# Kernel tuning notes

Measured on AMD Instinct MI355X. Metric: run time of the kernel, lower is better.

Reference implementation:

```python
import jax, jax.numpy as jnp
import numpy as np

N = 10000      # num_nodes
RP = 16        # latent relations
E = 64         # emb_dim
R = 8000       # num triples (MLP input dim)
NT = 8000      # unique (s,o) pairs (unique by construction)
LW = 64        # lwidth
C = 16         # num_classes
NREL = 50      # num_rels (<= R columns actually used in nhots)


def setup_inputs() -> dict:
    rng = np.random.default_rng(0)
    # unique (s,o) pairs -> nt == R, deterministic shapes
    pair_ids = rng.choice(N * N, size=R, replace=False)
    s = (pair_ids // N).astype(np.int32)
    o = (pair_ids % N).astype(np.int32)
    p = rng.integers(0, NREL, size=R)
    nhots = np.zeros((NT, R), np.float32)
    nhots[np.arange(NT), p] = 1.0
    # replicate index construction from __init__ exactly
    rm = np.arange(RP, dtype=np.int32)[:, None]           # (RP,1)
    s_exp = np.broadcast_to(s[None, :], (RP, NT)).reshape(-1)
    o_exp = np.broadcast_to(o[None, :], (RP, NT)).reshape(-1)
    se = (s[None, :] * rm).reshape(-1)
    oe = (o[None, :] * rm).reshape(-1)
    hindices = np.stack([s_exp, oe], axis=1).astype(np.int32)  # into (N, N*RP)
    vindices = np.stack([se, o_exp], axis=1).astype(np.int32)  # into (N*RP, N)

    key = jax.random.key(0)
    ks = jax.random.split(key, 6)
    inv = lambda d: 1.0 / np.sqrt(d)
    return {
        'nhots': jnp.asarray(nhots),
        'w1a': jax.random.normal(ks[0], (R, LW), jnp.float32) * inv(R),
        'b1a': jnp.zeros((LW,), jnp.float32),
        'w1b': jax.random.normal(ks[1], (LW, RP), jnp.float32) * inv(LW),
        'b1b': jnp.zeros((RP,), jnp.float32),
        'w2a': jax.random.normal(ks[2], (R, LW), jnp.float32) * inv(R),
        'b2a': jnp.zeros((LW,), jnp.float32),
        'w2b': jax.random.normal(ks[3], (LW, RP), jnp.float32) * inv(LW),
        'b2b': jnp.zeros((RP,), jnp.float32),
        'weights1': jax.random.normal(ks[4], (RP, N, E), jnp.float32) * 0.02,
        'bias1': jnp.zeros((E,), jnp.float32),
        'weights2': jax.random.normal(ks[5], (RP, E, C), jnp.float32) * 0.02,
        'bias2': jnp.zeros((C,), jnp.float32),
        'hindices': jnp.asarray(hindices),
        'vindices': jnp.asarray(vindices),
    }


def _latents(nhots, wa, ba, wb, bb):
    # Linear -> ReLU -> Linear -> softmax over rp, then .t().reshape(-1)
    lat = jax.nn.softmax(jax.nn.relu(nhots @ wa + ba) @ wb + bb, axis=1)  # (NT, RP)
    return lat.T.reshape(-1)  # (RP*NT,) — rm-major, matching index construction


def reference(nhots, w1a, b1a, w1b, b1b, w2a, b2a, w2b, b2b,
              weights1, bias1, weights2, bias2, hindices, vindices):
    hrow, hcol = hindices[:, 0], hindices[:, 1]
    vrow, vcol = vindices[:, 0], vindices[:, 1]

    # --- layer 1: A1 (N, N*RP), column-normalized ---
    lat1 = _latents(nhots, w1a, b1a, w1b, b1b)
    colsum = jax.ops.segment_sum(lat1, hcol, num_segments=N * RP)
    lat1 = lat1 / colsum[hcol]
    Xw = weights1.reshape(RP * N, E)
    h = jax.ops.segment_sum(lat1[:, None] * Xw[hcol], hrow, num_segments=N)  # (N, E)
    h = jax.nn.relu(h + bias1)

    # --- layer 2: A2 (N*RP, N), row-normalized ---
    lat2 = _latents(nhots, w2a, b2a, w2b, b2b)
    rowsum = jax.ops.segment_sum(lat2, vrow, num_segments=N * RP)
    lat2 = lat2 / rowsum[vrow]
    h2 = jax.ops.segment_sum(lat2[:, None] * h[vcol], vrow, num_segments=N * RP)
    h2 = h2.reshape(RP, N, E)

    out = jnp.einsum('rhc,rnh->nc', weights2, h2) + bias2  # (N, C)
    return out
```

## Files before the change

### kernel.cpp

```cpp
#include <hip/hip_runtime.h>
#include <hip/hip_bf16.h>


#define N_     10000
#define RP_    16
#define E_     64
#define R_     8000
#define NT_    8000
#define C_     16
#define NE_    128000

#define WS_ZERO_UNITS 330064

__global__ void k_init_out(float* __restrict__ out, const float* __restrict__ bias2) {
    int i = blockIdx.x * 256 + threadIdx.x;
    out[i] = bias2[i & 15];
}

__global__ void k_lat(const float* __restrict__ nhots,
                      const float* __restrict__ w1a, const float* __restrict__ b1a,
                      const float* __restrict__ w1b, const float* __restrict__ b1b,
                      const float* __restrict__ w2a, const float* __restrict__ b2a,
                      const float* __restrict__ w2b, const float* __restrict__ b2b,
                      const int* __restrict__ hind, const int* __restrict__ vind,
                      float* __restrict__ lat1t, float* __restrict__ lat2,
                      float* __restrict__ colsum, float* __restrict__ rowsum,
                      int* __restrict__ cnt) {
    __shared__ float zb[4][128];
    __shared__ float r0[2];
    const int lane = threadIdx.x & 63;
    const int wv   = threadIdx.x >> 6;
    const int t    = blockIdx.x * 4 + wv;

    const float4 v = reinterpret_cast<const float4*>(nhots + (size_t)t * R_)[lane];
    float acc1 = 0.f, acc2 = 0.f;
    const float comp[4] = {v.x, v.y, v.z, v.w};
    #pragma unroll
    for (int c = 0; c < 4; ++c) {
        unsigned long long m = __ballot(comp[c] != 0.0f);
        while (m) {
            const int src = __ffsll(m) - 1;
            m &= m - 1;
            const float val = __shfl(comp[c], src);
            const int col = src * 4 + c;
            acc1 += val * w1a[col * 64 + lane];
            acc2 += val * w2a[col * 64 + lane];
        }
    }
    if (threadIdx.x == 0) { r0[0] = 0.f; r0[1] = 0.f; }
    zb[wv][lane]      = fmaxf(acc1 + b1a[lane], 0.f);
    zb[wv][64 + lane] = fmaxf(acc2 + b2a[lane], 0.f);
    __syncthreads();

    const int g = lane >> 4, r = lane & 15;
    float pre = 0.f;
    if (g < 2) {
        const float* wb = (g == 0) ? w1b : w2b;
        pre = ((g == 0) ? b1b : b2b)[r];
        const float* z = &zb[wv][g * 64];
        #pragma unroll
        for (int l = 0; l < 64; ++l) pre += z[l] * wb[l * 16 + r];
    }
    float mx = pre;
    #pragma unroll
    for (int m = 8; m >= 1; m >>= 1) mx = fmaxf(mx, __shfl_xor(mx, m, 16));
    const float e = expf(pre - mx);
    float s = e;
    #pragma unroll
    for (int m = 8; m >= 1; m >>= 1) s += __shfl_xor(s, m, 16);
    const float lt = e / s;

    const int s_t = hind[2 * t];
    const int o_t = vind[2 * t + 1];
    if (g == 0) {
        lat1t[t * 16 + r] = lt;
        if (r) atomicAdd(colsum + o_t * r, lt);
        else   atomicAdd(&r0[0], lt);
    } else if (g == 1) {
        lat2[r * NT_ + t] = lt;
        if (r) atomicAdd(rowsum + s_t * r, lt);
        else   atomicAdd(&r0[1], lt);
    } else if (g == 2 && r == 0) {
        atomicAdd(cnt + s_t, 1);
    }
    __syncthreads();
    if (threadIdx.x == 0) atomicAdd(colsum, r0[0]);
    if (threadIdx.x == 1) atomicAdd(rowsum, r0[1]);
}

__global__ void k_scan(const int* __restrict__ cnt, int* __restrict__ off,
                       int* __restrict__ woff) {
    __shared__ int sh[1024];
    const int i = threadIdx.x;
    int local[10];
    int sum = 0;
    const int base = i * 10;
    #pragma unroll
    for (int j = 0; j < 10; ++j) {
        const int idx = base + j;
        const int c = (idx < N_) ? cnt[idx] : 0;
        local[j] = c; sum += c;
    }
    sh[i] = sum;
    __syncthreads();
    for (int d = 1; d < 1024; d <<= 1) {
        const int v = (i >= d) ? sh[i - d] : 0;
        __syncthreads();
        sh[i] += v;
        __syncthreads();
    }
    int run = sh[i] - sum;
    #pragma unroll
    for (int j = 0; j < 10; ++j) {
        const int idx = base + j;
        if (idx < N_) { off[idx] = run; woff[idx] = run; run += local[j]; }
    }
    if (i == 1023) off[N_] = sh[1023];
}

__global__ void k_scatter(const int* __restrict__ hind, int* __restrict__ woff,
                          int* __restrict__ order) {
    const int t = blockIdx.x * 64 + threadIdx.x;
    const int n = hind[2 * t];
    const int pos = atomicAdd(woff + n, 1);
    order[pos] = t;
}

__global__ void k_hg(const float* __restrict__ lat1t, const float* __restrict__ colsum,
                     const int* __restrict__ off, const int* __restrict__ order,
                     const int* __restrict__ vind, const float* __restrict__ w1,
                     const float* __restrict__ bias1, float* __restrict__ hbuf) {
    const int lane = threadIdx.x & 63;
    const int n = blockIdx.x * 4 + (threadIdx.x >> 6);
    const int j1 = off[n + 1];
    float acc = 0.f;
    for (int j = off[n]; j < j1; ++j) {
        const int t = order[j];
        const int o_t = vind[2 * t + 1];
        float ln = 0.f;
        if (lane < 16) ln = lat1t[t * 16 + lane] / colsum[o_t * lane];
        #pragma unroll
        for (int r = 0; r < 16; ++r) {
            const float a = __shfl(ln, r);
            acc += a * w1[(o_t * r) * 64 + lane];
        }
    }
    hbuf[n * 64 + lane] = fmaxf(acc + bias1[lane], 0.f);
}

__global__ void k_h2r0(const float* __restrict__ lat2, const float* __restrict__ rowsum,
                       const int* __restrict__ vind, const float* __restrict__ hbuf,
                       float* __restrict__ h2r0) {
    const int l  = threadIdx.x & 63;
    const int wg = blockIdx.x * 4 + (threadIdx.x >> 6);
    float acc = 0.f;
    for (int t = wg; t < NT_; t += 256) {
        const int vc = vind[2 * t + 1];
        acc += lat2[t] * hbuf[vc * 64 + l];
    }
    acc /= rowsum[0];
    atomicAdd(&h2r0[l], acc);
}

__global__ void k_h2r0b(const float* __restrict__ h2r0, const float* __restrict__ w2,
                        float* __restrict__ out) {
    const int c = threadIdx.x;
    if (c < 16) {
        float acc = 0.f;
        #pragma unroll
        for (int hh = 0; hh < 64; ++hh) acc += w2[hh * 16 + c] * h2r0[hh];
        atomicAdd(&out[c], acc);
    }
}

__global__ void k_h2out(const float* __restrict__ lat2, const float* __restrict__ rowsum,
                        const int* __restrict__ vind, const float* __restrict__ hbuf,
                        const float* __restrict__ w2, float* __restrict__ out) {
    __shared__ float sw2[16384];
    for (int i = threadIdx.x; i < 16384; i += 256) sw2[i] = w2[i];
    __syncthreads();
    const int grp = (threadIdx.x >> 4) & 3;
    for (int gid = blockIdx.x * 256 + threadIdx.x; gid < 120000 * 16; gid += gridDim.x * 256) {
        const int e = gid >> 4;
        const int c = gid & 15;
        const int k = NT_ + e;
        const int q  = vind[2 * k];
        const int vc = vind[2 * k + 1];
        const float val = lat2[k] / rowsum[q];
        const int rp = q / N_;
        const int np = q - rp * N_;
        const float* wrow = &sw2[rp * 1024 + c];
        const float* hrow = &hbuf[vc * 64];
        float acc = 0.f;
        for (int hh = grp; hh < 64; ++hh) acc += wrow[hh * 16] * hrow[hh];
        for (int hh = 0; hh < grp; ++hh)  acc += wrow[hh * 16] * hrow[hh];
        atomicAdd(&out[np * 16 + c], val * acc);
    }
}

extern "C" void kernel_launch(void* const* d_in, const int* in_sizes, int n_in,
                              void* d_out, int out_size, void* d_ws, size_t ws_size,
                              hipStream_t stream) {
    const float* nhots    = (const float*)d_in[0];
    const float* w1a      = (const float*)d_in[1];
    const float* b1a      = (const float*)d_in[2];
    const float* w1b      = (const float*)d_in[3];
    const float* b1b      = (const float*)d_in[4];
    const float* w2a      = (const float*)d_in[5];
    const float* b2a      = (const float*)d_in[6];
    const float* w2b      = (const float*)d_in[7];
    const float* b2b      = (const float*)d_in[8];
    const float* weights1 = (const float*)d_in[9];
    const float* bias1    = (const float*)d_in[10];
    const float* weights2 = (const float*)d_in[11];
    const float* bias2    = (const float*)d_in[12];
    const int*   hind     = (const int*)d_in[13];
    const int*   vind     = (const int*)d_in[14];
    float* out = (float*)d_out;

    float* ws     = (float*)d_ws;
    float* colsum = ws;
    float* rowsum = ws + 160000;
    float* h2r0   = ws + 320000;
    int*   cnt    = (int*)(ws + 320064);
    int*   off    = (int*)(ws + 330064);
    int*   woff   = (int*)(ws + 340065);
    int*   order  = (int*)(ws + 350065);
    float* hbuf   = ws + 358080;
    float* lat1t  = ws + 998080;
    float* lat2   = ws + 1126080;

    hipMemsetAsync(d_ws, 0, WS_ZERO_UNITS * sizeof(float), stream);
    k_init_out<<<625, 256, 0, stream>>>(out, bias2);
    k_lat<<<2000, 256, 0, stream>>>(nhots, w1a, b1a, w1b, b1b, w2a, b2a, w2b, b2b,
                                    hind, vind, lat1t, lat2, colsum, rowsum, cnt);
    k_scan<<<1, 1024, 0, stream>>>(cnt, off, woff);
    k_scatter<<<125, 64, 0, stream>>>(hind, woff, order);
    k_hg<<<2500, 256, 0, stream>>>(lat1t, colsum, off, order, vind, weights1, bias1, hbuf);
    k_h2r0<<<64, 256, 0, stream>>>(lat2, rowsum, vind, hbuf, h2r0);
    k_h2out<<<1024, 256, 0, stream>>>(lat2, rowsum, vind, hbuf, weights2, out);
    k_h2r0b<<<1, 64, 0, stream>>>(h2r0, weights2, out);
}
```

Baseline: 515.5 us.

## Fuse small kernels and restructure layer-2 edge output to wave-per-edge shuffles

Folds output bias initialization into the latent kernel, merges the counting-sort scatter into the scan kernel using a shared-memory offset array, and combines the rp=0 reduction with the edge-output kernel in one launch. The edge kernel now assigns one wavefront per edge: each lane loads one h element, shuffles it across lanes for the 64x16 matvec, and reduces across quarters, so one atomic is issued per output class instead of 16 threads each reading the full h row. This aims to cut launch count and redundant global loads, at the cost of serializing the scatter in a single block and adding shuffle work.

```diff
diff --git a/kernel.cpp b/kernel.cpp
--- a/kernel.cpp
+++ b/kernel.cpp
@@ -11,11 +11,6 @@
 #define NE_    128000
 
 #define WS_ZERO_UNITS 330064
-
-__global__ void k_init_out(float* __restrict__ out, const float* __restrict__ bias2) {
-    int i = blockIdx.x * 256 + threadIdx.x;
-    out[i] = bias2[i & 15];
-}
 
 __global__ void k_lat(const float* __restrict__ nhots,
                       const float* __restrict__ w1a, const float* __restrict__ b1a,
@@ -25,12 +20,18 @@
                       const int* __restrict__ hind, const int* __restrict__ vind,
                       float* __restrict__ lat1t, float* __restrict__ lat2,
                       float* __restrict__ colsum, float* __restrict__ rowsum,
-                      int* __restrict__ cnt) {
+                      int* __restrict__ cnt,
+                      float* __restrict__ out, const float* __restrict__ bias2) {
     __shared__ float zb[4][128];
     __shared__ float r0[2];
     const int lane = threadIdx.x & 63;
     const int wv   = threadIdx.x >> 6;
     const int t    = blockIdx.x * 4 + wv;
+
+    if (threadIdx.x < 80) {
+        const int i = blockIdx.x * 80 + threadIdx.x;
+        out[i] = bias2[i & 15];
+    }
 
     const float4 v = reinterpret_cast<const float4*>(nhots + (size_t)t * R_)[lane];
     float acc1 = 0.f, acc2 = 0.f;
@@ -89,8 +90,9 @@
 }
 
 __global__ void k_scan(const int* __restrict__ cnt, int* __restrict__ off,
-                       int* __restrict__ woff) {
+                       const int* __restrict__ hind, int* __restrict__ order) {
     __shared__ int sh[1024];
+    __shared__ int woff[N_];
     const int i = threadIdx.x;
     int local[10];
     int sum = 0;
@@ -116,14 +118,12 @@
         if (idx < N_) { off[idx] = run; woff[idx] = run; run += local[j]; }
     }
     if (i == 1023) off[N_] = sh[1023];
-}
-
-__global__ void k_scatter(const int* __restrict__ hind, int* __restrict__ woff,
-                          int* __restrict__ order) {
-    const int t = blockIdx.x * 64 + threadIdx.x;
-    const int n = hind[2 * t];
-    const int pos = atomicAdd(woff + n, 1);
-    order[pos] = t;
+    __syncthreads();
+    for (int t = i; t < NT_; t += 1024) {
+        const int n = hind[2 * t];
+        const int pos = atomicAdd(&woff[n], 1);
+        order[pos] = t;
+    }
 }
 
 __global__ void k_hg(const float* __restrict__ lat1t, const float* __restrict__ colsum,
@@ -148,18 +148,50 @@
     hbuf[n * 64 + lane] = fmaxf(acc + bias1[lane], 0.f);
 }
 
-__global__ void k_h2r0(const float* __restrict__ lat2, const float* __restrict__ rowsum,
-                       const int* __restrict__ vind, const float* __restrict__ hbuf,
-                       float* __restrict__ h2r0) {
-    const int l  = threadIdx.x & 63;
-    const int wg = blockIdx.x * 4 + (threadIdx.x >> 6);
-    float acc = 0.f;
-    for (int t = wg; t < NT_; t += 256) {
-        const int vc = vind[2 * t + 1];
-        acc += lat2[t] * hbuf[vc * 64 + l];
-    }
-    acc /= rowsum[0];
-    atomicAdd(&h2r0[l], acc);
+__global__ void k_h2all(const float* __restrict__ lat2, const float* __restrict__ rowsum,
+                        const int* __restrict__ vind, const float* __restrict__ hbuf,
+                        const float* __restrict__ w2, float* __restrict__ out,
+                        float* __restrict__ h2r0) {
+    const int lane = threadIdx.x & 63;
+    const int wv   = threadIdx.x >> 6;
+
+    if (blockIdx.x >= 512) {
+        const int wg = (blockIdx.x - 512) * 4 + wv;
+        float acc = 0.f;
+        for (int t = wg; t < NT_; t += 256) {
+            const int vc = vind[2 * t + 1];
+            acc += lat2[t] * hbuf[vc * 64 + lane];
+        }
+        acc /= rowsum[0];
+        atomicAdd(&h2r0[lane], acc);
+        return;
+    }
+
+    __shared__ float sw2[16384];
+    for (int i = threadIdx.x; i < 16384; i += 256) sw2[i] = w2[i];
+    __syncthreads();
+
+    const int c = lane & 15;
+    const int quarter = lane >> 4;
+    for (int e = blockIdx.x * 4 + wv; e < 120000; e += 512 * 4) {
+        const int k  = NT_ + e;
+        const int q  = vind[2 * k];
+        const int vc = vind[2 * k + 1];
+        const float val = lat2[k] / rowsum[q];
+        const int rp = q / N_;
+        const int np = q - rp * N_;
+        const float u = val * hbuf[vc * 64 + lane];
+        float partial = 0.f;
+        #pragma unroll
+        for (int j = 0; j < 16; ++j) {
+            const int hh = quarter * 16 + ((j + quarter) & 15);
+            const float hv = __shfl(u, hh);
+            partial += hv * sw2[rp * 1024 + hh * 16 + c];
+        }
+        partial += __shfl_xor(partial, 16);
+        partial += __shfl_xor(partial, 32);
+        if (quarter == 0) atomicAdd(&out[np * 16 + c], partial);
+    }
 }
 
 __global__ void k_h2r0b(const float* __restrict__ h2r0, const float* __restrict__ w2,
@@ -170,31 +202,6 @@
         #pragma unroll
         for (int hh = 0; hh < 64; ++hh) acc += w2[hh * 16 + c] * h2r0[hh];
         atomicAdd(&out[c], acc);
-    }
-}
-
-__global__ void k_h2out(const float* __restrict__ lat2, const float* __restrict__ rowsum,
-                        const int* __restrict__ vind, const float* __restrict__ hbuf,
-                        const float* __restrict__ w2, float* __restrict__ out) {
-    __shared__ float sw2[16384];
-    for (int i = threadIdx.x; i < 16384; i += 256) sw2[i] = w2[i];
-    __syncthreads();
-    const int grp = (threadIdx.x >> 4) & 3;
-    for (int gid = blockIdx.x * 256 + threadIdx.x; gid < 120000 * 16; gid += gridDim.x * 256) {
-        const int e = gid >> 4;
-        const int c = gid & 15;
-        const int k = NT_ + e;
-        const int q  = vind[2 * k];
-        const int vc = vind[2 * k + 1];
-        const float val = lat2[k] / rowsum[q];
-        const int rp = q / N_;
-        const int np = q - rp * N_;
-        const float* wrow = &sw2[rp * 1024 + c];
-        const float* hrow = &hbuf[vc * 64];
-        float acc = 0.f;
-        for (int hh = grp; hh < 64; ++hh) acc += wrow[hh * 16] * hrow[hh];
-        for (int hh = 0; hh < grp; ++hh)  acc += wrow[hh * 16] * hrow[hh];
-        atomicAdd(&out[np * 16 + c], val * acc);
     }
 }
 
@@ -224,20 +231,17 @@
     float* h2r0   = ws + 320000;
     int*   cnt    = (int*)(ws + 320064);
     int*   off    = (int*)(ws + 330064);
-    int*   woff   = (int*)(ws + 340065);
     int*   order  = (int*)(ws + 350065);
     float* hbuf   = ws + 358080;
     float* lat1t  = ws + 998080;
     float* lat2   = ws + 1126080;
 
     hipMemsetAsync(d_ws, 0, WS_ZERO_UNITS * sizeof(float), stream);
-    k_init_out<<<625, 256, 0, stream>>>(out, bias2);
     k_lat<<<2000, 256, 0, stream>>>(nhots, w1a, b1a, w1b, b1b, w2a, b2a, w2b, b2b,
-                                    hind, vind, lat1t, lat2, colsum, rowsum, cnt);
-    k_scan<<<1, 1024, 0, stream>>>(cnt, off, woff);
-    k_scatter<<<125, 64, 0, stream>>>(hind, woff, order);
+                                    hind, vind, lat1t, lat2, colsum, rowsum, cnt,
+                                    out, bias2);
+    k_scan<<<1, 1024, 0, stream>>>(cnt, off, hind, order);
     k_hg<<<2500, 256, 0, stream>>>(lat1t, colsum, off, order, vind, weights1, bias1, hbuf);
-    k_h2r0<<<64, 256, 0, stream>>>(lat2, rowsum, vind, hbuf, h2r0);
-    k_h2out<<<1024, 256, 0, stream>>>(lat2, rowsum, vind, hbuf, weights2, out);
+    k_h2all<<<576, 256, 0, stream>>>(lat2, rowsum, vind, hbuf, weights2, out, h2r0);
     k_h2r0b<<<1, 64, 0, stream>>>(h2r0, weights2, out);
 }
```

After: 466.9 us. -9.4%, faster.
